# Kernel tuning notes

Hardware: AMD Instinct MI355X
Metric: run time of the kernel (lower is better)

The kernel has to match this reference:

```python
import jax, jax.numpy as jnp
import numpy as np

B, T = 128, 512
V, E, U, K = 50000, 100, 128, 32


def _lstm(x, Wk, Wr, b):
    # x: [B, T, D] -> [B, T, U], Keras LSTM gate order i,f,g,o
    Bd = x.shape[0]
    Ud = Wr.shape[0]
    xs = jnp.swapaxes(x, 0, 1)  # [T, B, D]

    def step(carry, xt):
        h, c = carry
        z = xt @ Wk + h @ Wr + b
        i, f, g, o = jnp.split(z, 4, axis=-1)
        c = jax.nn.sigmoid(f) * c + jax.nn.sigmoid(i) * jnp.tanh(g)
        h = jax.nn.sigmoid(o) * jnp.tanh(c)
        return (h, c), h

    init = (jnp.zeros((Bd, Ud), x.dtype), jnp.zeros((Bd, Ud), x.dtype))
    _, hs = jax.lax.scan(step, init, xs)
    return jnp.swapaxes(hs, 0, 1)


def _crf_logZ(em, trans):
    # em: [B, T, K] emissions; trans: [K, K]. Forward algorithm log-partition.
    alpha0 = em[:, 0]  # [B, K]
    es = jnp.swapaxes(em[:, 1:], 0, 1)  # [T-1, B, K]

    def step(alpha, et):
        # alpha[b, i] + trans[i, j] -> logsumexp over i, plus emission
        alpha = jax.nn.logsumexp(alpha[:, :, None] + trans[None], axis=1) + et
        return alpha, None

    alphaT, _ = jax.lax.scan(step, alpha0, es)
    return jax.nn.logsumexp(alphaT, axis=-1)  # [B]


def setup_inputs() -> dict:
    key = jax.random.key(0)
    ks = jax.random.split(key, 11)
    s = 0.1
    return {
        "tokens": jax.random.randint(ks[0], (B, T), 0, V, dtype=jnp.int32),
        "emb": jax.random.normal(ks[1], (V, E), jnp.float32) * s,
        "Wk_f": jax.random.normal(ks[2], (E, 4 * U), jnp.float32) * s,
        "Wr_f": jax.random.normal(ks[3], (U, 4 * U), jnp.float32) * s,
        "b_f": jnp.zeros((4 * U,), jnp.float32),
        "Wk_b": jax.random.normal(ks[4], (E, 4 * U), jnp.float32) * s,
        "Wr_b": jax.random.normal(ks[5], (U, 4 * U), jnp.float32) * s,
        "b_b": jnp.zeros((4 * U,), jnp.float32),
        "crf_kernel": jax.random.normal(ks[6], (2 * U, K), jnp.float32) * s,
        "crf_bias": jnp.zeros((K,), jnp.float32),
        "trans": jax.random.normal(ks[7], (K, K), jnp.float32) * s,
    }


def reference(tokens, emb, Wk_f, Wr_f, b_f, Wk_b, Wr_b, b_b, crf_kernel, crf_bias, trans):
    x = emb[tokens]  # [B, T, E]
    h_f = _lstm(x, Wk_f, Wr_f, b_f)
    h_b = _lstm(x[:, ::-1], Wk_b, Wr_b, b_b)[:, ::-1]
    h = jnp.concatenate([h_f, h_b], axis=-1)  # [B, T, 2U] (dropout = identity at inference)
    em = h @ crf_kernel + crf_bias  # [B, T, K] CRF emission potentials
    return _crf_logZ(em, trans)  # [B] log-partition via CRF forward DP
```

## Files before the change

### kernel.cpp

```cpp
#include <hip/hip_runtime.h>
#include <hip/hip_bf16.h>

#define B_  128
#define T_  512
#define V_  50000
#define VP  50016
#define E_  100
#define U_  128
#define K_  32
#define G4  512
#define KP  128
#define GRP 8

typedef _Float16 h2_t __attribute__((ext_vector_type(2)));
typedef _Float16 f16x8 __attribute__((ext_vector_type(8)));
typedef __fp16   h2raw_t __attribute__((ext_vector_type(2)));
typedef short    bf16x8 __attribute__((ext_vector_type(8)));
typedef float    f32x4  __attribute__((ext_vector_type(4)));

__device__ __forceinline__ h2_t pk2(float a, float b) {
    h2raw_t r = __builtin_amdgcn_cvt_pkrtz(a, b);
    union { h2raw_t r; h2_t h; } u; u.r = r; return u.h;
}
__device__ __forceinline__ int h2_as_int(h2_t v) { union { h2_t h; int i; } u; u.h = v; return u.i; }

#if __has_builtin(__builtin_amdgcn_rcpf)
__device__ __forceinline__ float rcp_f(float x) { return __builtin_amdgcn_rcpf(x); }
#else
__device__ __forceinline__ float rcp_f(float x) { return 1.f / x; }
#endif

__device__ __forceinline__ unsigned short bf16_bits(float v) {
    __hip_bfloat16 b = __float2bfloat16(v);
    union { __hip_bfloat16 b; unsigned short s; } u; u.b = b; return u.s;
}

__global__ __launch_bounds__(128) void pack_b_kernel(
    const float* __restrict__ Wk_f, const float* __restrict__ Wk_b,
    __hip_bfloat16* __restrict__ Bb)
{
    const int n = blockIdx.x;
    const int k = threadIdx.x;
    float v = 0.f;
    if (k < E_) v = (n < 512) ? Wk_f[k * 512 + n] : Wk_b[k * 512 + (n - 512)];
    Bb[n * KP + k] = __float2bfloat16(v);
}

__global__ __launch_bounds__(256, 2) void proj_mfma_kernel(
    const float* __restrict__ emb,
    const __hip_bfloat16* __restrict__ Bb,
    const float* __restrict__ b_f, const float* __restrict__ b_b,
    __hip_bfloat16* __restrict__ proj)
{
    const int r0   = blockIdx.x * 32;
    const int tid  = threadIdx.x;
    const int wv   = tid >> 6;
    const int lane = tid & 63;
    const int quad = lane >> 4;
    const int l16  = lane & 15;

    __shared__ __align__(16) float C_lds[32][268];
    unsigned short* A_st = (unsigned short*)&C_lds[0][0];

    for (int idx = tid; idx < 32 * 64; idx += 256) {
        int r = idx >> 6, kk = idx & 63;
        int vr = r0 + r; if (vr >= V_) vr = V_ - 1;
        unsigned int w = 0;
        if (kk < 50) {
            float2 v = *(const float2*)(emb + (long long)vr * E_ + 2 * kk);
            w = ((unsigned int)bf16_bits(v.y) << 16) | bf16_bits(v.x);
        }
        *(unsigned int*)&A_st[r * 136 + 2 * kk] = w;
    }
    __syncthreads();

    bf16x8 af[2][4];
    #pragma unroll
    for (int mt = 0; mt < 2; ++mt)
        #pragma unroll
        for (int kc = 0; kc < 4; ++kc)
            af[mt][kc] = *(const bf16x8*)&A_st[(mt * 16 + l16) * 136 +
                                               kc * 32 + quad * 8];
    __syncthreads();

    const unsigned short* Bu = (const unsigned short*)Bb;

    for (int ng = 0; ng < 4; ++ng) {
        const int n0 = ng * 256;

        bf16x8 bfr[4][4];
        #pragma unroll
        for (int nt = 0; nt < 4; ++nt)
            #pragma unroll
            for (int kc = 0; kc < 4; ++kc)
                bfr[nt][kc] = *(const bf16x8*)(Bu +
                    (n0 + wv * 64 + nt * 16 + l16) * KP + kc * 32 + quad * 8);

        f32x4 acc[2][4];
        #pragma unroll
        for (int mt = 0; mt < 2; ++mt)
            #pragma unroll
            for (int nt = 0; nt < 4; ++nt)
                acc[mt][nt] = (f32x4){0.f, 0.f, 0.f, 0.f};

        #pragma unroll
        for (int mt = 0; mt < 2; ++mt)
            #pragma unroll
            for (int nt = 0; nt < 4; ++nt)
                #pragma unroll
                for (int kc = 0; kc < 4; ++kc)
                    acc[mt][nt] = __builtin_amdgcn_mfma_f32_16x16x32_bf16(
                        af[mt][kc], bfr[nt][kc], acc[mt][nt], 0, 0, 0);

        #pragma unroll
        for (int mt = 0; mt < 2; ++mt)
            #pragma unroll
            for (int nt = 0; nt < 4; ++nt)
                #pragma unroll
                for (int v = 0; v < 4; ++v)
                    C_lds[mt * 16 + quad * 4 + v][wv * 64 + nt * 16 + l16] =
                        acc[mt][nt][v];
        __syncthreads();

        const float* bias = (n0 < 512) ? b_f : b_b;
        const int nbase = n0 & 511;
        for (int idx = tid; idx < 32 * 128; idx += 256) {
            int r = idx >> 7, cc = (idx & 127) * 2;
            float v0 = C_lds[r][cc]     + bias[nbase + cc];
            float v1 = C_lds[r][cc + 1] + bias[nbase + cc + 1];
            unsigned int w = ((unsigned int)bf16_bits(v1) << 16) | bf16_bits(v0);
            *(unsigned int*)(proj + (long long)(r0 + r) * 1024 + n0 + cc) = w;
        }
        __syncthreads();
    }
}

__device__ __forceinline__ float sigmoid_f(float x) {
    return rcp_f(1.f + __expf(-x));
}
__device__ __forceinline__ float tanh_f(float x) {
    return 1.f - 2.f * rcp_f(__expf(2.f * x) + 1.f);
}

__global__ __launch_bounds__(512, 1) void lstm_kernel(
    const __hip_bfloat16* __restrict__ proj,
    const int* __restrict__ tokens,
    const float* __restrict__ Wr_f, const float* __restrict__ Wr_b,
    __hip_bfloat16* __restrict__ h_buf)
{
    const int bid  = blockIdx.x;
    const int dir  = bid >> 7;
    const int b    = bid & 127;
    const int tid  = threadIdx.x;
    const int w    = tid >> 6;
    const int lane = tid & 63;
    const int quad = lane >> 4;
    const int l16  = lane & 15;
    const int unit = 16 * w + l16;

    const float* Wr = dir ? Wr_b : Wr_f;

    union uf16 { f16x8 v; h2_t p[4]; };
    f16x8 wb[4][4];
    #pragma unroll
    for (int gq = 0; gq < 4; ++gq) {
        const int col = gq * 128 + unit;
        #pragma unroll
        for (int kc = 0; kc < 4; ++kc) {
            const int k0 = kc * 32 + quad * 8;
            uf16 u;
            #pragma unroll
            for (int jj = 0; jj < 4; ++jj)
                u.p[jj] = pk2(Wr[(k0 + 2 * jj)     * G4 + col],
                              Wr[(k0 + 2 * jj + 1) * G4 + col]);
            wb[gq][kc] = u.v;
        }
    }

    __shared__ __align__(16) _Float16 hpl[2][128];
    if (tid < 128) hpl[0][tid] = (_Float16)0.f;
    float c = 0.f;
    __syncthreads();

    const int tbase = b * T_;
    const long long rowbase = (long long)b * T_;
    const __hip_bfloat16* pr = proj + dir * 512 + unit;

    int tok_cur[GRP], tok_nxt[GRP];
    #pragma unroll
    for (int d = 0; d < GRP; ++d) {
        int t0 = dir ? (T_ - 1 - d) : d;
        tok_cur[d] = tokens[tbase + t0];
        int t1 = dir ? (T_ - 1 - (GRP + d)) : (GRP + d);
        tok_nxt[d] = tokens[tbase + t1];
    }

    float xk_cur[GRP][4];
    #pragma unroll
    for (int d = 0; d < GRP; ++d)
        #pragma unroll
        for (int g = 0; g < 4; ++g)
            xk_cur[d][g] = __bfloat162float(
                pr[(long long)tok_cur[d] * 1024 + g * 128]);

    unsigned int hpack[GRP];
    #pragma unroll
    for (int d = 0; d < GRP; ++d) hpack[d] = 0;

    for (int g = 0; g < T_ / GRP; ++g) {
        float xk_nxt[GRP][4];
        #pragma unroll
        for (int d = 0; d < GRP; ++d)
            #pragma unroll
            for (int gg = 0; gg < 4; ++gg) xk_nxt[d][gg] = 0.f;
        if (g + 1 < T_ / GRP) {
            #pragma unroll
            for (int d = 0; d < GRP; ++d)
                #pragma unroll
                for (int gg = 0; gg < 4; ++gg)
                    xk_nxt[d][gg] = __bfloat162float(
                        pr[(long long)tok_nxt[d] * 1024 + gg * 128]);
        }
        int tok_n2[GRP];
        #pragma unroll
        for (int d = 0; d < GRP; ++d) tok_n2[d] = 0;
        if (g + 2 < T_ / GRP) {
            #pragma unroll
            for (int d = 0; d < GRP; ++d) {
                int s = (g + 2) * GRP + d;
                int t = dir ? (T_ - 1 - s) : s;
                tok_n2[d] = tokens[tbase + t];
            }
        }

        #pragma unroll
        for (int d = 0; d < GRP; ++d) {
            f16x8 a[4];
            #pragma unroll
            for (int kc = 0; kc < 4; ++kc)
                a[kc] = *(const f16x8*)&hpl[d & 1][kc * 32 + quad * 8];

            f32x4 acc[4];
            #pragma unroll
            for (int gq = 0; gq < 4; ++gq)
                acc[gq] = (f32x4){0.f, 0.f, 0.f, 0.f};
            #pragma unroll
            for (int gq = 0; gq < 4; ++gq)
                #pragma unroll
                for (int kc = 0; kc < 4; ++kc)
                    acc[gq] = __builtin_amdgcn_mfma_f32_16x16x32_f16(
                        a[kc], wb[gq][kc], acc[gq], 0, 0, 0);

            float zi = acc[0][0] + xk_cur[d][0];
            float zf = acc[1][0] + xk_cur[d][1];
            float zg = acc[2][0] + xk_cur[d][2];
            float zo = acc[3][0] + xk_cur[d][3];
            c = sigmoid_f(zf) * c + sigmoid_f(zi) * tanh_f(zg);
            float h = sigmoid_f(zo) * tanh_f(c);

            if (quad == 0) hpl[(d + 1) & 1][unit] = (_Float16)h;

            float hn = __shfl_down(h, 1, 64);
            if (quad == 0 && !(l16 & 1))
                hpack[d] = ((unsigned int)bf16_bits(hn) << 16) | bf16_bits(h);

            __syncthreads();
        }

        if (quad == 0 && !(l16 & 1)) {
            #pragma unroll
            for (int d = 0; d < GRP; ++d) {
                int s = g * GRP + d;
                int t = dir ? (T_ - 1 - s) : s;
                *(unsigned int*)(h_buf + (rowbase + t) * 256 + dir * U_ + unit) =
                    hpack[d];
            }
        }

        #pragma unroll
        for (int d = 0; d < GRP; ++d) {
            #pragma unroll
            for (int gg = 0; gg < 4; ++gg) xk_cur[d][gg] = xk_nxt[d][gg];
            tok_nxt[d] = tok_n2[d];
        }
    }
}

__global__ __launch_bounds__(256) void em_kernel(
    const __hip_bfloat16* __restrict__ h_buf,
    const float* __restrict__ ck, const float* __restrict__ cb,
    float* __restrict__ em)
{
    const int tid  = threadIdx.x;
    const int part = tid >> 5;
    const int k    = tid & 31;

    float ckr[32];
    #pragma unroll
    for (int i = 0; i < 32; ++i)
        ckr[i] = ck[(part * 32 + i) * K_ + k];
    const float cbk = cb[k];

    __shared__ float h_l[8][256];
    __shared__ float part_l[8][8][K_];

    const int r0 = blockIdx.x * 64;

    for (int round = 0; round < 8; ++round) {
        const int rbase = r0 + round * 8;
        #pragma unroll
        for (int j = 0; j < 8; ++j)
            h_l[j][tid] = __bfloat162float(h_buf[(long long)(rbase + j) * 256 + tid]);
        __syncthreads();

        #pragma unroll
        for (int j = 0; j < 8; ++j) {
            float pp = 0.f;
            #pragma unroll
            for (int i = 0; i < 32; ++i)
                pp = fmaf(h_l[j][part * 32 + i], ckr[i], pp);
            part_l[j][part][k] = pp;
        }
        __syncthreads();

        {
            int j2 = tid >> 5;
            float e = cbk;
            #pragma unroll
            for (int pq = 0; pq < 8; ++pq) e += part_l[j2][pq][k];
            em[(long long)(rbase + j2) * K_ + k] = e;
        }
        __syncthreads();
    }
}

#define PF_ 8
__global__ __launch_bounds__(64) void crf_kernel(
    const float* __restrict__ em,
    const float* __restrict__ trans,
    float* __restrict__ out)
{
    const int b    = blockIdx.x;
    const int lane = threadIdx.x;
    const int k    = lane & 31;
    const int half = lane >> 5;

    float etr[16];
    #pragma unroll
    for (int i = 0; i < 16; ++i)
        etr[i] = __expf(trans[(half * 16 + i) * K_ + k]);

    const float* em_b = em + (long long)b * T_ * K_;

    float ep[PF_];
    #pragma unroll
    for (int d = 0; d < PF_; ++d)
        ep[d] = em_b[d * K_ + k];

    float w = 0.f;
    float L = 0.f;
    for (int tb = 0; tb < T_; tb += PF_) {
        float en[PF_];
        if (tb + PF_ < T_) {
            #pragma unroll
            for (int d = 0; d < PF_; ++d)
                en[d] = em_b[(tb + PF_ + d) * K_ + k];
        } else {
            #pragma unroll
            for (int d = 0; d < PF_; ++d) en[d] = 0.f;
        }

        float eem[PF_];
        #pragma unroll
        for (int d = 0; d < PF_; ++d) eem[d] = __expf(ep[d]);

        #pragma unroll
        for (int d = 0; d < PF_; ++d) {
            if (tb + d == 0) {
                w = eem[d];
            } else {
                float acc = 0.f;
                #pragma unroll
                for (int i = 0; i < 16; ++i) {
                    float wv = __shfl(w, half * 16 + i, 64);
                    acc = fmaf(wv, etr[i], acc);
                }
                acc += __shfl_xor(acc, 32, 64);
                w = acc * eem[d];
            }
        }

        {
            float w0 = __shfl(w, 0, 64);
            w *= rcp_f(w0);
            L += __logf(w0);
        }

        #pragma unroll
        for (int d = 0; d < PF_; ++d) ep[d] = en[d];
    }

    float s = w;
    #pragma unroll
    for (int d = 1; d < 32; d <<= 1)
        s += __shfl_xor(s, d, 64);
    if (lane == 0) out[b] = L + __logf(s);
}

extern "C" void kernel_launch(void* const* d_in, const int* in_sizes, int n_in,
                              void* d_out, int out_size, void* d_ws, size_t ws_size,
                              hipStream_t stream)
{
    const int*   tokens = (const int*)  d_in[0];
    const float* emb    = (const float*)d_in[1];
    const float* Wk_f   = (const float*)d_in[2];
    const float* Wr_f   = (const float*)d_in[3];
    const float* b_f    = (const float*)d_in[4];
    const float* Wk_b   = (const float*)d_in[5];
    const float* Wr_b   = (const float*)d_in[6];
    const float* b_b    = (const float*)d_in[7];
    const float* ck     = (const float*)d_in[8];
    const float* cb     = (const float*)d_in[9];
    const float* trans  = (const float*)d_in[10];
    float* out = (float*)d_out;

    const long long ROWS = (long long)B_ * T_;
    __hip_bfloat16* proj  = (__hip_bfloat16*)d_ws;
    __hip_bfloat16* h_buf = proj + (long long)VP * 1024;
    float* em = (float*)(h_buf + ROWS * 256);
    __hip_bfloat16* Bb = (__hip_bfloat16*)(em + ROWS * K_);

    hipLaunchKernelGGL(pack_b_kernel, dim3(1024), dim3(128), 0, stream,
                       Wk_f, Wk_b, Bb);
    hipLaunchKernelGGL(proj_mfma_kernel, dim3(VP / 32), dim3(256), 0, stream,
                       emb, Bb, b_f, b_b, proj);
    hipLaunchKernelGGL(lstm_kernel, dim3(256), dim3(512), 0, stream,
                       proj, tokens, Wr_f, Wr_b, h_buf);
    hipLaunchKernelGGL(em_kernel, dim3((int)(ROWS / 64)), dim3(256), 0, stream,
                       h_buf, ck, cb, em);
    hipLaunchKernelGGL(crf_kernel, dim3(B_), dim3(64), 0, stream,
                       em, trans, out);
}
```

Baseline: 597.4 us.

## Stage LSTM input projections through double-buffered LDS with cooperative gather

Instead of each thread loading its own four gate projections for every timestep from global memory, all 512 threads gather one bf16 value each per timestep into a double-buffered shared-memory staging array, and each lane reads back four packed values with one vector LDS load. __syncthreads is replaced by an explicit lgkmcnt wait plus s_barrier. The shuffle and bf16 packing of hidden outputs move out of the per-step critical path to the end of each group. This cuts register pressure and redundant gathers in the serial recurrence, at the cost of extra LDS traffic and a manual barrier that depends on correct wait counts.

```diff
diff --git a/kernel.cpp b/kernel.cpp
--- a/kernel.cpp
+++ b/kernel.cpp
@@ -17,12 +17,12 @@
 typedef __fp16   h2raw_t __attribute__((ext_vector_type(2)));
 typedef short    bf16x8 __attribute__((ext_vector_type(8)));
 typedef float    f32x4  __attribute__((ext_vector_type(4)));
+typedef unsigned short u16x4 __attribute__((ext_vector_type(4)));
 
 __device__ __forceinline__ h2_t pk2(float a, float b) {
     h2raw_t r = __builtin_amdgcn_cvt_pkrtz(a, b);
     union { h2raw_t r; h2_t h; } u; u.r = r; return u.h;
 }
-__device__ __forceinline__ int h2_as_int(h2_t v) { union { h2_t h; int i; } u; u.h = v; return u.i; }
 
 #if __has_builtin(__builtin_amdgcn_rcpf)
 __device__ __forceinline__ float rcp_f(float x) { return __builtin_amdgcn_rcpf(x); }
@@ -33,6 +33,9 @@
 __device__ __forceinline__ unsigned short bf16_bits(float v) {
     __hip_bfloat16 b = __float2bfloat16(v);
     union { __hip_bfloat16 b; unsigned short s; } u; u.b = b; return u.s;
+}
+__device__ __forceinline__ float bf2f(unsigned short u) {
+    union { unsigned int i; float f; } x; x.i = ((unsigned int)u) << 16; return x.f;
 }
 
 __global__ __launch_bounds__(128) void pack_b_kernel(
@@ -178,67 +181,60 @@
     }
 
     __shared__ __align__(16) _Float16 hpl[2][128];
+    __shared__ __align__(16) unsigned short xkl[2][GRP][512];
     if (tid < 128) hpl[0][tid] = (_Float16)0.f;
     float c = 0.f;
-    __syncthreads();
 
     const int tbase = b * T_;
     const long long rowbase = (long long)b * T_;
-    const __hip_bfloat16* pr = proj + dir * 512 + unit;
-
-    int tok_cur[GRP], tok_nxt[GRP];
-    #pragma unroll
-    for (int d = 0; d < GRP; ++d) {
-        int t0 = dir ? (T_ - 1 - d) : d;
-        tok_cur[d] = tokens[tbase + t0];
-        int t1 = dir ? (T_ - 1 - (GRP + d)) : (GRP + d);
-        tok_nxt[d] = tokens[tbase + t1];
-    }
-
-    float xk_cur[GRP][4];
-    #pragma unroll
-    for (int d = 0; d < GRP; ++d)
-        #pragma unroll
-        for (int g = 0; g < 4; ++g)
-            xk_cur[d][g] = __bfloat162float(
-                pr[(long long)tok_cur[d] * 1024 + g * 128]);
-
-    unsigned int hpack[GRP];
-    #pragma unroll
-    for (int d = 0; d < GRP; ++d) hpack[d] = 0;
-
-    for (int g = 0; g < T_ / GRP; ++g) {
-        float xk_nxt[GRP][4];
+    const __hip_bfloat16* prt = proj + dir * 512 + tid;
+    const int xw = (tid & 127) * 4 + (tid >> 7);
+
+    int tokn[GRP];
+    {
+        unsigned short v0[GRP];
+        #pragma unroll
+        for (int d = 0; d < GRP; ++d) {
+            int t0 = dir ? (T_ - 1 - d) : d;
+            int tk = tokens[tbase + t0];
+            v0[d] = *(const unsigned short*)(prt + (long long)tk * 1024);
+        }
         #pragma unroll
         for (int d = 0; d < GRP; ++d)
-            #pragma unroll
-            for (int gg = 0; gg < 4; ++gg) xk_nxt[d][gg] = 0.f;
-        if (g + 1 < T_ / GRP) {
-            #pragma unroll
-            for (int d = 0; d < GRP; ++d)
-                #pragma unroll
-                for (int gg = 0; gg < 4; ++gg)
-                    xk_nxt[d][gg] = __bfloat162float(
-                        pr[(long long)tok_nxt[d] * 1024 + gg * 128]);
-        }
-        int tok_n2[GRP];
-        #pragma unroll
-        for (int d = 0; d < GRP; ++d) tok_n2[d] = 0;
-        if (g + 2 < T_ / GRP) {
-            #pragma unroll
-            for (int d = 0; d < GRP; ++d) {
-                int s = (g + 2) * GRP + d;
-                int t = dir ? (T_ - 1 - s) : s;
-                tok_n2[d] = tokens[tbase + t];
-            }
-        }
-
+            xkl[0][d][xw] = v0[d];
+        #pragma unroll
+        for (int d = 0; d < GRP; ++d) {
+            int s = GRP + d;
+            int t1 = dir ? (T_ - 1 - s) : s;
+            tokn[d] = tokens[tbase + t1];
+        }
+    }
+    __syncthreads();
+
+    const int NG = T_ / GRP;
+    for (int g = 0; g < NG; ++g) {
+        unsigned short xknx[GRP];
+        #pragma unroll
+        for (int d = 0; d < GRP; ++d)
+            xknx[d] = *(const unsigned short*)(prt + (long long)tokn[d] * 1024);
+
+        int tokn2[GRP];
+        #pragma unroll
+        for (int d = 0; d < GRP; ++d) {
+            int s = (g + 2) * GRP + d; if (s > T_ - 1) s = T_ - 1;
+            int t = dir ? (T_ - 1 - s) : s;
+            tokn2[d] = tokens[tbase + t];
+        }
+
+        float hreg[GRP];
         #pragma unroll
         for (int d = 0; d < GRP; ++d) {
             f16x8 a[4];
             #pragma unroll
             for (int kc = 0; kc < 4; ++kc)
                 a[kc] = *(const f16x8*)&hpl[d & 1][kc * 32 + quad * 8];
+
+            u16x4 xr = *(const u16x4*)&xkl[g & 1][d][(unsigned)unit * 4];
 
             f32x4 acc[4];
             #pragma unroll
@@ -251,38 +247,48 @@
                     acc[gq] = __builtin_amdgcn_mfma_f32_16x16x32_f16(
                         a[kc], wb[gq][kc], acc[gq], 0, 0, 0);
 
-            float zi = acc[0][0] + xk_cur[d][0];
-            float zf = acc[1][0] + xk_cur[d][1];
-            float zg = acc[2][0] + xk_cur[d][2];
-            float zo = acc[3][0] + xk_cur[d][3];
+            float zi = acc[0][0] + bf2f(xr.x);
+            float zf = acc[1][0] + bf2f(xr.y);
+            float zg = acc[2][0] + bf2f(xr.z);
+            float zo = acc[3][0] + bf2f(xr.w);
             c = sigmoid_f(zf) * c + sigmoid_f(zi) * tanh_f(zg);
             float h = sigmoid_f(zo) * tanh_f(c);
+            hreg[d] = h;
 
             if (quad == 0) hpl[(d + 1) & 1][unit] = (_Float16)h;
 
-            float hn = __shfl_down(h, 1, 64);
-            if (quad == 0 && !(l16 & 1))
-                hpack[d] = ((unsigned int)bf16_bits(hn) << 16) | bf16_bits(h);
-
-            __syncthreads();
-        }
-
+            if (d < GRP - 1) {
+                asm volatile("s_waitcnt lgkmcnt(0)" ::: "memory");
+                __builtin_amdgcn_s_barrier();
+                asm volatile("" ::: "memory");
+            } else {
+                #pragma unroll
+                for (int dd = 0; dd < GRP; ++dd)
+                    xkl[(g + 1) & 1][dd][xw] = xknx[dd];
+                asm volatile("s_waitcnt lgkmcnt(0)" ::: "memory");
+                __builtin_amdgcn_s_barrier();
+                asm volatile("" ::: "memory");
+            }
+        }
+
+        unsigned int hp[GRP];
+        #pragma unroll
+        for (int d = 0; d < GRP; ++d) {
+            float hn = __shfl_down(hreg[d], 1, 64);
+            hp[d] = ((unsigned int)bf16_bits(hn) << 16) | bf16_bits(hreg[d]);
+        }
         if (quad == 0 && !(l16 & 1)) {
             #pragma unroll
             for (int d = 0; d < GRP; ++d) {
                 int s = g * GRP + d;
                 int t = dir ? (T_ - 1 - s) : s;
                 *(unsigned int*)(h_buf + (rowbase + t) * 256 + dir * U_ + unit) =
-                    hpack[d];
+                    hp[d];
             }
         }
 
         #pragma unroll
-        for (int d = 0; d < GRP; ++d) {
-            #pragma unroll
-            for (int gg = 0; gg < 4; ++gg) xk_cur[d][gg] = xk_nxt[d][gg];
-            tok_nxt[d] = tok_n2[d];
-        }
+        for (int d = 0; d < GRP; ++d) tokn[d] = tokn2[d];
     }
 }
 
```

New measurement: 575.7 us. 1.04x faster.
